# Optimization experiments

Measured on AMD Instinct MI355X. Metric: run time of the kernel, lower is better.

The kernel has to match this reference:

```python
import jax, jax.numpy as jnp
import numpy as np

# ---- fixed architecture hyperparameters (match init_kwargs) ----
B, S = 4, 1024
L, H, DM, DF = 4, 8, 512, 2048
DH = DM // H          # 64 head dim (= 2*R after gated SPE filter)
NS = 5                # num_sines
R = 32                # num_realizations
M = 2 * DH            # favor_feature_dims = 128 (split as +/- of 64 projections)
LN_EPS = 1e-5
ATT_EPS = 1e-6


def layernorm(x, g, b):
    mu = x.mean(-1, keepdims=True)
    var = ((x - mu) ** 2).mean(-1, keepdims=True)
    return (x - mu) * jax.lax.rsqrt(var + LN_EPS) * g + b


def sine_spe(freqs, offsets, gains, noise, seq_len):
    """SineSPE positional code. freqs/offsets/gains: (H,DH,NS); noise: (H,DH,2NS,R).
    Returns qbar, kbar of shape (S,H,DH,R)."""
    pos = jnp.arange(seq_len, dtype=freqs.dtype)
    f = jax.nn.sigmoid(freqs)[:, :, None, :] / 2.0                       # (H,DH,1,NS)
    ph_q = 2.0 * jnp.pi * f * pos[None, None, :, None] + offsets[:, :, None, :]
    ph_k = 2.0 * jnp.pi * f * pos[None, None, :, None]
    om_q = jnp.stack([jnp.cos(ph_q), jnp.sin(ph_q)], -1).reshape(H, DH, seq_len, 2 * NS)
    om_k = jnp.stack([jnp.cos(ph_k), jnp.sin(ph_k)], -1).reshape(H, DH, seq_len, 2 * NS)
    g = jax.nn.softplus(gains)
    g = jnp.stack([g, g], -1).reshape(H, DH, 2 * NS)                      # upsample gains
    z = noise * g[..., None] / jnp.sqrt(jnp.asarray(2.0 * NS, freqs.dtype))
    qbar = jnp.einsum('hdsk,hdkr->shdr', om_q, z)
    kbar = jnp.einsum('hdsk,hdkr->shdr', om_k, z)
    scale = (R * DH) ** 0.25
    return qbar / scale, kbar / scale


def spe_filter(q, k, qbar, kbar, gate, gnoise):
    """Gated SPE filter. q,k: (B,S,H,DH); qbar/kbar: (S,H,DH,R); gate: (H,DH); gnoise: (H,DH,R).
    Returns qhat, khat of shape (B,S,H,2R)."""
    g = jax.nn.sigmoid(gate)[..., None]                                   # (H,DH,1)
    gn = gnoise / (DH * R) ** 0.25
    seq_len = qbar.shape[0]
    bias = jnp.broadcast_to(jnp.sqrt(g) * gn, (seq_len, H, DH, R))
    qb = jnp.concatenate([jnp.sqrt(1.0 - g) * qbar, bias], -1)            # (S,H,DH,2R)
    kb = jnp.concatenate([jnp.sqrt(1.0 - g) * kbar, bias], -1)
    qhat = jnp.einsum('bshd,shdr->bshr', q, qb)
    khat = jnp.einsum('bshd,shdr->bshr', k, kb)
    return qhat, khat


def favor(x, omega):
    """FAVOR+ softmax feature map. x: (B,S,H,DH); omega: (DH, M//2) -> (B,S,H,M)."""
    x = x * (DH ** -0.25)                                                 # sqrt(softmax_temp), temp=1/sqrt(DH)
    half_norm = 0.5 * jnp.sum(x * x, -1, keepdims=True)
    u = jnp.einsum('bshe,em->bshm', x, omega)
    phi = jnp.concatenate([jnp.exp(u - half_norm), jnp.exp(-u - half_norm)], -1)
    return phi / jnp.sqrt(jnp.asarray(M, x.dtype))


def causal_linear_attention(Q, K, V):
    """Causal linear (kernelized) attention via lax.scan. Q,K: (B,S,H,M); V: (B,S,H,DH)."""
    Bv = Q.shape[0]

    def step(carry, qkv):
        Skv, sk = carry
        q, k, v = qkv                                                     # (B,H,M),(B,H,M),(B,H,DH)
        Skv = Skv + jnp.einsum('bhm,bhd->bhmd', k, v)
        sk = sk + k
        num = jnp.einsum('bhm,bhmd->bhd', q, Skv)
        den = jnp.einsum('bhm,bhm->bh', q, sk) + ATT_EPS
        return (Skv, sk), num / den[..., None]

    init = (jnp.zeros((Bv, H, M, DH), Q.dtype), jnp.zeros((Bv, H, M), Q.dtype))
    xs = tuple(jnp.moveaxis(t, 1, 0) for t in (Q, K, V))
    _, out = jax.lax.scan(step, init, xs)
    return jnp.moveaxis(out, 0, 1)                                        # (B,S,H,DH)


def setup_inputs() -> dict:
    key = jax.random.key(0)
    ks = jax.random.split(key, 14)

    def rn(k, shape, scale=1.0):
        return jax.random.normal(k, shape, dtype=jnp.float32) * scale

    return {
        'x': rn(ks[0], (B, S, DM)),
        'Wq': rn(ks[1], (L, DM, DM), 0.02), 'bq': jnp.zeros((L, DM), jnp.float32),
        'Wk': rn(ks[2], (L, DM, DM), 0.02), 'bk': jnp.zeros((L, DM), jnp.float32),
        'Wv': rn(ks[3], (L, DM, DM), 0.02), 'bv': jnp.zeros((L, DM), jnp.float32),
        'Wo': rn(ks[4], (L, DM, DM), 0.02), 'bo': jnp.zeros((L, DM), jnp.float32),
        'W1': rn(ks[5], (L, DM, DF), 0.02), 'b1': jnp.zeros((L, DF), jnp.float32),
        'W2': rn(ks[6], (L, DF, DM), 0.02), 'b2': jnp.zeros((L, DM), jnp.float32),
        'ln1_g': jnp.ones((L, DM), jnp.float32), 'ln1_b': jnp.zeros((L, DM), jnp.float32),
        'ln2_g': jnp.ones((L, DM), jnp.float32), 'ln2_b': jnp.zeros((L, DM), jnp.float32),
        'spe_freqs': rn(ks[7], (L, H, DH, NS)),
        'spe_offsets': rn(ks[8], (L, H, DH, NS)),
        'spe_gains': rn(ks[9], (L, H, DH, NS)),
        'spe_noise': rn(ks[10], (L, H, DH, 2 * NS, R)),
        'gate': rn(ks[11], (L, H, DH)),
        'gate_noise': rn(ks[12], (L, H, DH, R)),
        'favor_omega': rn(ks[13], (L, DH, M // 2)),
    }


def reference(x, Wq, bq, Wk, bk, Wv, bv, Wo, bo, W1, b1, W2, b2,
              ln1_g, ln1_b, ln2_g, ln2_b,
              spe_freqs, spe_offsets, spe_gains, spe_noise, gate, gate_noise, favor_omega):
    Bv, Sv, _ = x.shape
    out = x
    for l in range(L):
        qbar, kbar = sine_spe(spe_freqs[l], spe_offsets[l], spe_gains[l], spe_noise[l], Sv)
        q = (out @ Wq[l] + bq[l]).reshape(Bv, Sv, H, DH)
        k = (out @ Wk[l] + bk[l]).reshape(Bv, Sv, H, DH)
        v = (out @ Wv[l] + bv[l]).reshape(Bv, Sv, H, DH)
        qh, kh = spe_filter(q, k, qbar, kbar, gate[l], gate_noise[l])
        Qf = favor(qh, favor_omega[l])
        Kf = favor(kh, favor_omega[l])
        att = causal_linear_attention(Qf, Kf, v).reshape(Bv, Sv, DM)
        att = att @ Wo[l] + bo[l]
        h = layernorm(out + att, ln1_g[l], ln1_b[l])
        y = jax.nn.relu(h @ W1[l] + b1[l]) @ W2[l] + b2[l]
        out = layernorm(h + y, ln2_g[l], ln2_b[l])
    return out
```

## Files before the change

### kernel.cpp

```cpp
#include <hip/hip_runtime.h>
#include <math.h>

#define BB 4
#define SS 1024
#define LL 4
#define HH 8
#define DM 512
#define DF 2048
#define DH 64
#define NS 5
#define RR 32
#define MM 128
#define NC 16
#define CHK 64
#define QKV_N 1536

#define INV_SQRT10   0.316227766016838f
#define INV_SCALE    0.148650889375340f
#define TEMP_SCALE   0.353553390593274f
#define INV_SQRT_M   0.088388347648318f
#define TWO_PI       6.283185307179586f

typedef __attribute__((ext_vector_type(8))) short bf16x8;
typedef __attribute__((ext_vector_type(4))) float f32x4;

__device__ __forceinline__ unsigned short f2bf(float f) {
  union { float f; unsigned int u; } v; v.f = f;
  unsigned int r = v.u + 0x7FFFu + ((v.u >> 16) & 1u);
  return (unsigned short)(r >> 16);
}

__device__ __forceinline__ float bf2f(unsigned short u) {
  union { unsigned int u; float f; } v; v.u = (unsigned int)u << 16;
  return v.f;
}

__device__ __forceinline__ void gld_lds16(const unsigned short* g, unsigned short* l) {
  __builtin_amdgcn_global_load_lds((const __attribute__((address_space(1))) void*)g,
                                   (__attribute__((address_space(3))) void*)l,
                                   16, 0, 0);
}

template<int RELU, int OUT_BF>
__global__ __launch_bounds__(256)
void gemm_mfma(const unsigned short* __restrict__ A, const unsigned short* __restrict__ Bt,
               const float* __restrict__ bias, float* __restrict__ Cf,
               unsigned short* __restrict__ Cbf, int M, int N, int K)
{
  __shared__ unsigned short As[128 * 32];
  __shared__ unsigned short Bs[128 * 32];
  const int tid  = threadIdx.x;
  const int w    = tid >> 6;
  const int lane = tid & 63;
  const int row0 = blockIdx.y * 128;
  const int col0 = blockIdx.x * 128;
  const int wr = (w >> 1) * 64;
  const int wc = (w & 1) * 64;
  const int c0 = w * 2, c1 = w * 2 + 1;
  const int m0 = c0 * 16 + (lane >> 2);
  const int m1 = c1 * 16 + (lane >> 2);
  const int kA = (lane & 3) * 8;

  f32x4 acc[4][4] = {};

  for (int k0 = 0; k0 < K; k0 += 32) {
    gld_lds16(&A [(size_t)(row0 + m0) * K + k0 + kA], &As[c0 * 512]);
    gld_lds16(&A [(size_t)(row0 + m1) * K + k0 + kA], &As[c1 * 512]);
    gld_lds16(&Bt[(size_t)(col0 + m0) * K + k0 + kA], &Bs[c0 * 512]);
    gld_lds16(&Bt[(size_t)(col0 + m1) * K + k0 + kA], &Bs[c1 * 512]);
    __syncthreads();
    const int rA = wr + (lane & 15);
    const int rB = wc + (lane & 15);
    const int kk = (lane >> 4) * 8;
    bf16x8 af[4], bfr[4];
#pragma unroll
    for (int i = 0; i < 4; ++i) {
      af[i]  = *reinterpret_cast<const bf16x8*>(&As[(rA + i * 16) * 32 + kk]);
      bfr[i] = *reinterpret_cast<const bf16x8*>(&Bs[(rB + i * 16) * 32 + kk]);
    }
#pragma unroll
    for (int mi = 0; mi < 4; ++mi)
#pragma unroll
      for (int ni = 0; ni < 4; ++ni)
        acc[mi][ni] = __builtin_amdgcn_mfma_f32_16x16x32_bf16(af[mi], bfr[ni], acc[mi][ni], 0, 0, 0);
    __syncthreads();
  }
  const int cr = (lane >> 4) * 4;
  const int cc = lane & 15;
#pragma unroll
  for (int mi = 0; mi < 4; ++mi) {
#pragma unroll
    for (int ni = 0; ni < 4; ++ni) {
      const int col = col0 + wc + ni * 16 + cc;
      const float bv = bias[col];
#pragma unroll
      for (int r = 0; r < 4; ++r) {
        const int row = row0 + wr + mi * 16 + cr + r;
        float v = acc[mi][ni][r] + bv;
        if (RELU) v = fmaxf(v, 0.f);
        if (OUT_BF) Cbf[(size_t)row * N + col] = f2bf(v);
        else        Cf [(size_t)row * N + col] = v;
      }
    }
  }
}

template<int RELU, int OUT_BF>
__global__ __launch_bounds__(256)
void gemm_mfma_n64(const unsigned short* __restrict__ A, const unsigned short* __restrict__ Bt,
                   const float* __restrict__ bias, float* __restrict__ Cf,
                   unsigned short* __restrict__ Cbf, int M, int N, int K)
{
  __shared__ unsigned short As[128 * 32];
  __shared__ unsigned short Bs[64 * 32];
  const int tid  = threadIdx.x;
  const int w    = tid >> 6;
  const int lane = tid & 63;
  const int row0 = blockIdx.y * 128;
  const int col0 = blockIdx.x * 64;
  const int wr = (w >> 1) * 64;
  const int wc = (w & 1) * 32;
  const int c0 = w * 2, c1 = w * 2 + 1;
  const int m0 = c0 * 16 + (lane >> 2);
  const int m1 = c1 * 16 + (lane >> 2);
  const int mb = w * 16 + (lane >> 2);
  const int kA = (lane & 3) * 8;

  f32x4 acc[4][2] = {};

  for (int k0 = 0; k0 < K; k0 += 32) {
    gld_lds16(&A [(size_t)(row0 + m0) * K + k0 + kA], &As[c0 * 512]);
    gld_lds16(&A [(size_t)(row0 + m1) * K + k0 + kA], &As[c1 * 512]);
    gld_lds16(&Bt[(size_t)(col0 + mb) * K + k0 + kA], &Bs[w * 512]);
    __syncthreads();
    const int rA = wr + (lane & 15);
    const int rB = wc + (lane & 15);
    const int kk = (lane >> 4) * 8;
    bf16x8 af[4], bfr[2];
#pragma unroll
    for (int i = 0; i < 4; ++i)
      af[i]  = *reinterpret_cast<const bf16x8*>(&As[(rA + i * 16) * 32 + kk]);
#pragma unroll
    for (int i = 0; i < 2; ++i)
      bfr[i] = *reinterpret_cast<const bf16x8*>(&Bs[(rB + i * 16) * 32 + kk]);
#pragma unroll
    for (int mi = 0; mi < 4; ++mi)
#pragma unroll
      for (int ni = 0; ni < 2; ++ni)
        acc[mi][ni] = __builtin_amdgcn_mfma_f32_16x16x32_bf16(af[mi], bfr[ni], acc[mi][ni], 0, 0, 0);
    __syncthreads();
  }
  const int cr = (lane >> 4) * 4;
  const int cc = lane & 15;
#pragma unroll
  for (int mi = 0; mi < 4; ++mi) {
#pragma unroll
    for (int ni = 0; ni < 2; ++ni) {
      const int col = col0 + wc + ni * 16 + cc;
      const float bv = bias[col];
#pragma unroll
      for (int r = 0; r < 4; ++r) {
        const int row = row0 + wr + mi * 16 + cr + r;
        float v = acc[mi][ni][r] + bv;
        if (RELU) v = fmaxf(v, 0.f);
        if (OUT_BF) Cbf[(size_t)row * N + col] = f2bf(v);
        else        Cf [(size_t)row * N + col] = v;
      }
    }
  }
}

__global__ __launch_bounds__(256)
void transpose_bf(const float* __restrict__ W, unsigned short* __restrict__ Wt, int K, int N,
                  size_t inStride, size_t outStride)
{
  const float* Wl = W + blockIdx.z * inStride;
  unsigned short* Wtl = Wt + blockIdx.z * outStride;
  __shared__ float tile[32][33];
  const int k0 = blockIdx.y * 32, n0 = blockIdx.x * 32;
  const int tx = threadIdx.x & 31, ty = threadIdx.x >> 5;
#pragma unroll
  for (int j = 0; j < 4; ++j)
    tile[ty + 8 * j][tx] = Wl[(size_t)(k0 + ty + 8 * j) * N + n0 + tx];
  __syncthreads();
#pragma unroll
  for (int j = 0; j < 4; ++j)
    Wtl[(size_t)(n0 + ty + 8 * j) * K + k0 + tx] = f2bf(tile[tx][ty + 8 * j]);
}

__global__ __launch_bounds__(256)
void pack_bias(const float* __restrict__ bq, const float* __restrict__ bk,
               const float* __restrict__ bv, float* __restrict__ out)
{
  const int l = blockIdx.y;
  const int i = blockIdx.x * 256 + threadIdx.x;
  if (i < QKV_N)
    out[l * QKV_N + i] = (i < 512) ? bq[l * DM + i] : (i < 1024) ? bk[l * DM + i - 512]
                                                                 : bv[l * DM + i - 1024];
}

__global__ __launch_bounds__(256)
void cvt_bf16(const float* __restrict__ in, unsigned short* __restrict__ out, int n4)
{
  const int i = blockIdx.x * 256 + threadIdx.x;
  if (i < n4) {
    const float4 v = reinterpret_cast<const float4*>(in)[i];
    ushort4 o;
    o.x = f2bf(v.x); o.y = f2bf(v.y); o.z = f2bf(v.z); o.w = f2bf(v.w);
    reinterpret_cast<ushort4*>(out)[i] = o;
  }
}

__global__ __launch_bounds__(256)
void spe_prep_all(const float* __restrict__ gains, const float* __restrict__ noise,
                  const float* __restrict__ gate, const float* __restrict__ gnoise,
                  const float* __restrict__ offsets,
                  unsigned short* __restrict__ zpb, unsigned short* __restrict__ wbb,
                  float2* __restrict__ offcs)
{
  const int i = blockIdx.x * 256 + threadIdx.x;
  const int NZ = LL * HH * RR * 10 * DH;
  const int NW = LL * HH * RR * DH;
  const int NO = LL * HH * DH * NS;
  if (i < NZ) {
    const int d = i & 63;
    int j = i >> 6;
    const int k = j % 10; j /= 10;
    const int r = j & 31; j >>= 5;
    const int h = j & 7;  const int l = j >> 3;
    const int lhd = (l * HH + h) * DH + d;
    const float ga = gains[lhd * NS + (k >> 1)];
    const float sp = (ga > 20.f) ? ga : log1pf(__expf(ga));
    const float gg = 1.f / (1.f + __expf(-gate[lhd]));
    const float c1 = sqrtf(fmaxf(1.f - gg, 0.f));
    const float nz = noise[((size_t)lhd * 10 + k) * 32 + r];
    zpb[i] = f2bf(nz * sp * c1 * (INV_SQRT10 * INV_SCALE));
  } else if (i < NZ + NW) {
    int j = i - NZ;
    const int d = j & 63; j >>= 6;
    const int r = j & 31; j >>= 5;
    const int h = j & 7;  const int l = j >> 3;
    const int lhd = (l * HH + h) * DH + d;
    const float gg = 1.f / (1.f + __expf(-gate[lhd]));
    wbb[i - NZ] = f2bf(sqrtf(gg) * gnoise[(size_t)lhd * 32 + r] * INV_SCALE);
  } else if (i < NZ + NW + NO) {
    const int j = i - NZ - NW;
    float sn, cn;
    __sincosf(offsets[j], &sn, &cn);
    offcs[j] = make_float2(cn, sn);
  }
}

__global__ __launch_bounds__(256)
void spe_xhat(const float* __restrict__ freqs, const float2* __restrict__ offcs,
              const unsigned short* __restrict__ zpb, const unsigned short* __restrict__ wbb,
              const float* __restrict__ qkv,
              unsigned short* __restrict__ xhat, float* __restrict__ hn)
{
  const int s = blockIdx.x;
  const int h = blockIdx.y;
  const int t = threadIdx.x;
  const int w = t >> 6;
  const int lane = t & 63;
  __shared__ float omqT[10][64];
  __shared__ float omkT[10][64];
  __shared__ unsigned short qbT[64 * 64];
  __shared__ unsigned short kbT[64 * 64];
  __shared__ unsigned short rQ[16 * 64];
  __shared__ unsigned short rK[16 * 64];
  __shared__ float hqp[4][8];

  for (int e = t; e < DH * NS; e += 256) {
    const int d = e / NS, ns = e - d * NS;
    const float fr = 0.5f / (1.f + __expf(-freqs[(h * DH + d) * NS + ns]));
    float sn, cn;
    __sincosf(TWO_PI * fr * (float)s, &sn, &cn);
    const float2 oc = offcs[(h * DH + d) * NS + ns];
    omkT[2 * ns][d]     = cn;
    omkT[2 * ns + 1][d] = sn;
    omqT[2 * ns][d]     = cn * oc.x - sn * oc.y;
    omqT[2 * ns + 1][d] = sn * oc.x + cn * oc.y;
  }
  {
    const int b = t >> 6, d = t & 63;
    const size_t idx = ((size_t)b * SS + s) * QKV_N + h * DH + d;
    const int sd = d ^ ((b & 7) << 3);
    rQ[b * 64 + sd] = f2bf(qkv[idx] * TEMP_SCALE);
    rK[b * 64 + sd] = f2bf(qkv[idx + 512] * TEMP_SCALE);
  }
  for (int i = t; i < 768; i += 256) {
    rQ[256 + i] = 0;
    rK[256 + i] = 0;
  }
  __syncthreads();
  {
    const int r = t >> 3, dg = t & 7, d0 = dg * 8;
    float accq[8] = {}, acck[8] = {};
    const unsigned short* zr = zpb + (size_t)(h * RR + r) * 10 * 64 + d0;
#pragma unroll
    for (int k = 0; k < 10; ++k) {
      const bf16x8 zv = *reinterpret_cast<const bf16x8*>(zr + (size_t)k * 64);
      const float4 oq0 = *reinterpret_cast<const float4*>(&omqT[k][d0]);
      const float4 oq1 = *reinterpret_cast<const float4*>(&omqT[k][d0 + 4]);
      const float4 ok0 = *reinterpret_cast<const float4*>(&omkT[k][d0]);
      const float4 ok1 = *reinterpret_cast<const float4*>(&omkT[k][d0 + 4]);
      float zf[8];
#pragma unroll
      for (int j = 0; j < 8; ++j) zf[j] = bf2f((unsigned short)zv[j]);
      accq[0] += zf[0] * oq0.x; accq[1] += zf[1] * oq0.y;
      accq[2] += zf[2] * oq0.z; accq[3] += zf[3] * oq0.w;
      accq[4] += zf[4] * oq1.x; accq[5] += zf[5] * oq1.y;
      accq[6] += zf[6] * oq1.z; accq[7] += zf[7] * oq1.w;
      acck[0] += zf[0] * ok0.x; acck[1] += zf[1] * ok0.y;
      acck[2] += zf[2] * ok0.z; acck[3] += zf[3] * ok0.w;
      acck[4] += zf[4] * ok1.x; acck[5] += zf[5] * ok1.y;
      acck[6] += zf[6] * ok1.z; acck[7] += zf[7] * ok1.w;
    }
    bf16x8 qv, kv;
#pragma unroll
    for (int j = 0; j < 8; ++j) {
      qv[j] = (short)f2bf(accq[j]);
      kv[j] = (short)f2bf(acck[j]);
    }
    const int sd0 = d0 ^ ((r & 7) << 3);
    *reinterpret_cast<bf16x8*>(&qbT[r * 64 + sd0]) = qv;
    *reinterpret_cast<bf16x8*>(&kbT[r * 64 + sd0]) = kv;
    const bf16x8 wv = *reinterpret_cast<const bf16x8*>(&wbb[(size_t)(h * RR + r) * 64 + d0]);
    *reinterpret_cast<bf16x8*>(&qbT[(32 + r) * 64 + sd0]) = wv;
    *reinterpret_cast<bf16x8*>(&kbT[(32 + r) * 64 + sd0]) = wv;
  }
  __syncthreads();
  f32x4 aq = {0.f, 0.f, 0.f, 0.f}, ak = {0.f, 0.f, 0.f, 0.f};
  const int arow = lane & 15;
  const int colr = w * 16 + (lane & 15);
#pragma unroll
  for (int kt = 0; kt < 2; ++kt) {
    const int g = kt * 4 + (lane >> 4);
    const bf16x8 fAq = *reinterpret_cast<const bf16x8*>(&rQ[arow * 64 + ((g ^ (arow & 7)) << 3)]);
    const bf16x8 fAk = *reinterpret_cast<const bf16x8*>(&rK[arow * 64 + ((g ^ (arow & 7)) << 3)]);
    const bf16x8 fBq = *reinterpret_cast<const bf16x8*>(&qbT[colr * 64 + ((g ^ (colr & 7)) << 3)]);
    const bf16x8 fBk = *reinterpret_cast<const bf16x8*>(&kbT[colr * 64 + ((g ^ (colr & 7)) << 3)]);
    aq = __builtin_amdgcn_mfma_f32_16x16x32_bf16(fAq, fBq, aq, 0, 0, 0);
    ak = __builtin_amdgcn_mfma_f32_16x16x32_bf16(fAk, fBk, ak, 0, 0, 0);
  }
  float rq[4], rk2[4];
#pragma unroll
  for (int r = 0; r < 4; ++r) { rq[r] = aq[r] * aq[r]; rk2[r] = ak[r] * ak[r]; }
#pragma unroll
  for (int off = 1; off < 16; off <<= 1) {
#pragma unroll
    for (int r = 0; r < 4; ++r) {
      rq[r]  += __shfl_xor(rq[r],  off, 64);
      rk2[r] += __shfl_xor(rk2[r], off, 64);
    }
  }
  if (lane == 0) {
#pragma unroll
    for (int r = 0; r < 4; ++r) { hqp[w][r] = rq[r]; hqp[w][4 + r] = rk2[r]; }
  }
  if (lane < 16) {
#pragma unroll
    for (int r = 0; r < 4; ++r) {
      const size_t rowq = ((size_t)r * SS + s) * HH + h;
      xhat[rowq * 64 + w * 16 + lane] = f2bf(aq[r]);
      xhat[(rowq + (size_t)BB * SS * HH) * 64 + w * 16 + lane] = f2bf(ak[r]);
    }
  }
  __syncthreads();
  if (t < 8) {
    const int b = t & 3;
    const int ko = (t >> 2) * 4;
    const float v = 0.5f * (hqp[0][ko + b] + hqp[1][ko + b] + hqp[2][ko + b] + hqp[3][ko + b]);
    const size_t row = ((size_t)b * SS + s) * HH + h + (size_t)(t >> 2) * BB * SS * HH;
    hn[row] = v;
  }
}

__global__ __launch_bounds__(256)
void favor_gemm(const unsigned short* __restrict__ xhat, const unsigned short* __restrict__ omgT,
                const float* __restrict__ hn, unsigned short* __restrict__ QfKfB)
{
  __shared__ unsigned short As[128 * 32];
  __shared__ unsigned short Bs[64 * 32];
  const int tid  = threadIdx.x;
  const int w    = tid >> 6;
  const int lane = tid & 63;
  const int row0 = blockIdx.x * 128;
  const int c0 = w * 2, c1 = w * 2 + 1;
  const int m0 = c0 * 16 + (lane >> 2);
  const int m1 = c1 * 16 + (lane >> 2);
  const int mb = w * 16 + (lane >> 2);
  const int kA = (lane & 3) * 8;

  f32x4 acc[2][4] = {};

  for (int k0 = 0; k0 < 64; k0 += 32) {
    gld_lds16(&xhat[(size_t)(row0 + m0) * 64 + k0 + kA], &As[c0 * 512]);
    gld_lds16(&xhat[(size_t)(row0 + m1) * 64 + k0 + kA], &As[c1 * 512]);
    gld_lds16(&omgT[(size_t)mb * 64 + k0 + kA], &Bs[w * 512]);
    __syncthreads();
    const int rA = w * 32 + (lane & 15);
    const int kk = (lane >> 4) * 8;
    bf16x8 af[2], bfr[4];
#pragma unroll
    for (int i = 0; i < 2; ++i)
      af[i]  = *reinterpret_cast<const bf16x8*>(&As[(rA + i * 16) * 32 + kk]);
#pragma unroll
    for (int i = 0; i < 4; ++i)
      bfr[i] = *reinterpret_cast<const bf16x8*>(&Bs[(i * 16 + (lane & 15)) * 32 + kk]);
#pragma unroll
    for (int mi = 0; mi < 2; ++mi)
#pragma unroll
      for (int ni = 0; ni < 4; ++ni)
        acc[mi][ni] = __builtin_amdgcn_mfma_f32_16x16x32_bf16(af[mi], bfr[ni], acc[mi][ni], 0, 0, 0);
    __syncthreads();
  }
  const int cr = (lane >> 4) * 4;
  const int cc = lane & 15;
#pragma unroll
  for (int mi = 0; mi < 2; ++mi) {
#pragma unroll
    for (int r = 0; r < 4; ++r) {
      const size_t row = row0 + w * 32 + mi * 16 + cr + r;
      const float hnv = hn[row];
#pragma unroll
      for (int ni = 0; ni < 4; ++ni) {
        const int m = ni * 16 + cc;
        const float u = acc[mi][ni][r];
        QfKfB[row * MM + m]      = f2bf(__expf( u - hnv) * INV_SQRT_M);
        QfKfB[row * MM + m + 64] = f2bf(__expf(-u - hnv) * INV_SQRT_M);
      }
    }
  }
}

__global__ __launch_bounds__(256)
void attn_chunk_sums(const unsigned short* __restrict__ KfB, const float* __restrict__ qkv,
                     float* __restrict__ Sch, float* __restrict__ kch)
{
  const int c = blockIdx.x, h = blockIdx.y, b = blockIdx.z;
  const int tid = threadIdx.x;
  const int w = tid >> 6, lane = tid & 63;
  __shared__ unsigned short KcT[128 * 64];
  __shared__ unsigned short VT[64 * 64];
  const size_t srow0 = (size_t)b * SS + c * CHK;

  for (int i = tid; i < 8192; i += 256) {
    const int m = i & 127, t = i >> 7;
    KcT[m * 64 + (t ^ ((m & 7) << 3))] = KfB[((srow0 + t) * HH + h) * MM + m];
  }
  for (int i = tid; i < 4096; i += 256) {
    const int d = i & 63, tt = i >> 6;
    VT[d * 64 + (tt ^ ((d & 7) << 3))] = f2bf(qkv[(srow0 + tt) * QKV_N + 1024 + h * DH + d]);
  }
  __syncthreads();

  const int kk = (lane >> 4) * 8;
  f32x4 acc[2][4] = {};
#pragma unroll
  for (int kc = 0; kc < 2; ++kc) {
    const int k = kc * 32 + kk;
#pragma unroll
    for (int mi = 0; mi < 2; ++mi) {
      const int mA = w * 32 + mi * 16 + (lane & 15);
      const bf16x8 a = *reinterpret_cast<const bf16x8*>(&KcT[mA * 64 + (k ^ ((mA & 7) << 3))]);
#pragma unroll
      for (int ni = 0; ni < 4; ++ni) {
        const int dB = ni * 16 + (lane & 15);
        const bf16x8 bb = *reinterpret_cast<const bf16x8*>(&VT[dB * 64 + (k ^ ((dB & 7) << 3))]);
        acc[mi][ni] = __builtin_amdgcn_mfma_f32_16x16x32_bf16(a, bb, acc[mi][ni], 0, 0, 0);
      }
    }
  }
  const size_t base = (((size_t)b * HH + h) * NC + c);
  float* So = Sch + base * (MM * DH);
  const int cr = (lane >> 4) * 4, cc = lane & 15;
#pragma unroll
  for (int mi = 0; mi < 2; ++mi)
#pragma unroll
    for (int ni = 0; ni < 4; ++ni)
#pragma unroll
      for (int r = 0; r < 4; ++r)
        So[(size_t)(w * 32 + mi * 16 + cr + r) * DH + ni * 16 + cc] = acc[mi][ni][r];
  {
    const int m = tid >> 1, half = tid & 1;
    float ks = 0.f;
#pragma unroll
    for (int j = 0; j < 32; ++j) {
      const int t2 = half * 32 + j;
      ks += bf2f(KcT[m * 64 + (t2 ^ ((m & 7) << 3))]);
    }
    ks += __shfl_xor(ks, 1, 64);
    if (half == 0) kch[base * MM + m] = ks;
  }
}

__global__ __launch_bounds__(256)
void attn_scan(float* __restrict__ Sch, float* __restrict__ kch)
{
  const int bh = blockIdx.x, part = blockIdx.y;
  const int t = threadIdx.x;
  float* base = Sch + (size_t)bh * NC * (MM * DH);
  for (int e = part * 1024 + t; e < (part + 1) * 1024; e += 256) {
    float run = 0.f;
#pragma unroll
    for (int c = 0; c < NC; ++c) {
      const float v = base[(size_t)c * (MM * DH) + e];
      base[(size_t)c * (MM * DH) + e] = run;
      run += v;
    }
  }
  if (part == 0 && t < MM) {
    float* kb2 = kch + (size_t)bh * NC * MM;
    float run = 0.f;
#pragma unroll
    for (int c = 0; c < NC; ++c) {
      const float v = kb2[c * MM + t];
      kb2[c * MM + t] = run;
      run += v;
    }
  }
}

__global__ __launch_bounds__(256)
void attn_out(const unsigned short* __restrict__ QfKfB, const float* __restrict__ qkv,
              const float* __restrict__ Sch, const float* __restrict__ kch,
              unsigned short* __restrict__ att)
{
  const int c = blockIdx.x, h = blockIdx.y, b = blockIdx.z;
  const int tid = threadIdx.x;
  const int w = tid >> 6;
  const int lane = tid & 63;
  __shared__ unsigned short Qc[64 * 128];
  __shared__ unsigned short Sb[64 * 64];
  __shared__ unsigned short KVU[12288];
  __shared__ float skp[MM];
  __shared__ float denl[64];

  unsigned short* Kc   = KVU;
  unsigned short* SpxT = KVU;
  unsigned short* VT   = KVU + 8192;

  const size_t srow0 = (size_t)b * SS + c * CHK;
  const unsigned short* Qg = QfKfB + (srow0 * HH + h) * MM;
  const unsigned short* Kg = Qg + (size_t)BB * SS * HH * MM;

  if (tid < MM) skp[tid] = kch[(((size_t)b * HH + h) * NC + c) * MM + tid];

  for (int i = tid; i < 1024; i += 256) {
    const int s2 = i >> 4, m8 = (i & 15) * 8;
    const int sw = m8 ^ ((s2 & 15) << 3);
    *reinterpret_cast<bf16x8*>(&Qc[s2 * 128 + sw]) =
        *reinterpret_cast<const bf16x8*>(&Qg[(size_t)s2 * (HH * MM) + m8]);
    *reinterpret_cast<bf16x8*>(&Kc[s2 * 128 + sw]) =
        *reinterpret_cast<const bf16x8*>(&Kg[(size_t)s2 * (HH * MM) + m8]);
  }
  for (int i = tid; i < 4096; i += 256) {
    const int d = i & 63, tt = i >> 6;
    const float v = qkv[(srow0 + tt) * QKV_N + 1024 + h * DH + d];
    VT[d * 64 + (tt ^ ((d & 7) << 3))] = f2bf(v);
  }
  __syncthreads();

  const int sA = w * 16 + (lane & 15);
  const int kk = (lane >> 4) * 8;
  f32x4 acc_s[4] = {};
#pragma unroll
  for (int kc = 0; kc < 4; ++kc) {
    const int k = kc * 32 + kk;
    const bf16x8 aq = *reinterpret_cast<const bf16x8*>(&Qc[sA * 128 + (k ^ ((sA & 15) << 3))]);
#pragma unroll
    for (int n = 0; n < 4; ++n) {
      const int tB = n * 16 + (lane & 15);
      const bf16x8 bq = *reinterpret_cast<const bf16x8*>(&Kc[tB * 128 + (k ^ ((tB & 15) << 3))]);
      acc_s[n] = __builtin_amdgcn_mfma_f32_16x16x32_bf16(aq, bq, acc_s[n], 0, 0, 0);
    }
  }
  __syncthreads();

  {
    const int g = lane >> 4;
    const int tcol = lane & 15;
    float dintra[4] = {0.f, 0.f, 0.f, 0.f};
#pragma unroll
    for (int r = 0; r < 4; ++r) {
      const int s = w * 16 + g * 4 + r;
#pragma unroll
      for (int n = 0; n < 4; ++n) {
        const int t2 = n * 16 + tcol;
        const float v = (t2 <= s) ? acc_s[n][r] : 0.f;
        dintra[r] += v;
        Sb[s * 64 + (t2 ^ ((s & 7) << 3))] = f2bf(v);
      }
    }
#pragma unroll
    for (int off = 1; off < 16; off <<= 1)
#pragma unroll
      for (int r = 0; r < 4; ++r) dintra[r] += __shfl_xor(dintra[r], off, 64);
    if (tcol == 0) {
#pragma unroll
      for (int r = 0; r < 4; ++r) denl[w * 16 + g * 4 + r] = dintra[r];
    }
  }
  {
    const float* Sp = Sch + (((size_t)b * HH + h) * NC + c) * (MM * DH);
    for (int i = tid; i < 8192; i += 256) {
      const int d = i & 63, m = i >> 6;
      SpxT[d * 128 + (m ^ ((d & 15) << 3))] = f2bf(Sp[(size_t)m * DH + d]);
    }
  }
  __syncthreads();

  f32x4 acc_o[4] = {};
#pragma unroll
  for (int kc = 0; kc < 2; ++kc) {
    const int k = kc * 32 + kk;
    const bf16x8 as = *reinterpret_cast<const bf16x8*>(&Sb[sA * 64 + (k ^ ((sA & 7) << 3))]);
#pragma unroll
    for (int n = 0; n < 4; ++n) {
      const int dB = n * 16 + (lane & 15);
      const bf16x8 bv = *reinterpret_cast<const bf16x8*>(&VT[dB * 64 + (k ^ ((dB & 7) << 3))]);
      acc_o[n] = __builtin_amdgcn_mfma_f32_16x16x32_bf16(as, bv, acc_o[n], 0, 0, 0);
    }
  }
#pragma unroll
  for (int kc = 0; kc < 4; ++kc) {
    const int k = kc * 32 + kk;
    const bf16x8 aq = *reinterpret_cast<const bf16x8*>(&Qc[sA * 128 + (k ^ ((sA & 15) << 3))]);
#pragma unroll
    for (int n = 0; n < 4; ++n) {
      const int dB = n * 16 + (lane & 15);
      const bf16x8 bs = *reinterpret_cast<const bf16x8*>(&SpxT[dB * 128 + (k ^ ((dB & 15) << 3))]);
      acc_o[n] = __builtin_amdgcn_mfma_f32_16x16x32_bf16(aq, bs, acc_o[n], 0, 0, 0);
    }
  }
  {
    const int s2 = tid >> 2, part = tid & 3;
    float p = 0.f;
#pragma unroll
    for (int j = 0; j < 32; ++j) {
      const int m = part * 32 + j;
      p += bf2f(Qc[s2 * 128 + (m ^ ((s2 & 15) << 3))]) * skp[m];
    }
    p += __shfl_xor(p, 1, 64);
    p += __shfl_xor(p, 2, 64);
    if (part == 0) denl[s2] += p + 1e-6f;
  }
  __syncthreads();

  {
    const int g = lane >> 4;
    const int dcol = lane & 15;
#pragma unroll
    for (int r = 0; r < 4; ++r) {
      const int s = w * 16 + g * 4 + r;
      const float dinv = 1.f / denl[s];
#pragma unroll
      for (int n = 0; n < 4; ++n)
        att[(srow0 + s) * DM + h * DH + n * 16 + dcol] = f2bf(acc_o[n][r] * dinv);
    }
  }
}

template<int WBF>
__global__ __launch_bounds__(256)
void add_ln(const float* __restrict__ a, const float* __restrict__ bres,
            const float* __restrict__ g, const float* __restrict__ be,
            float* __restrict__ out, unsigned short* __restrict__ outbf)
{
  const int row = blockIdx.x;
  const int t = threadIdx.x;
  const size_t base = (size_t)row * DM;
  const float x0 = a[base + t] + bres[base + t];
  const float x1 = a[base + t + 256] + bres[base + t + 256];
  __shared__ float red[8];
  float ssum = x0 + x1;
#pragma unroll
  for (int off = 32; off > 0; off >>= 1) ssum += __shfl_xor(ssum, off, 64);
  const int wid = t >> 6, lid = t & 63;
  if (lid == 0) red[wid] = ssum;
  __syncthreads();
  const float mu = (red[0] + red[1] + red[2] + red[3]) * (1.f / DM);
  const float d0 = x0 - mu, d1 = x1 - mu;
  float sv = d0 * d0 + d1 * d1;
#pragma unroll
  for (int off = 32; off > 0; off >>= 1) sv += __shfl_xor(sv, off, 64);
  if (lid == 0) red[4 + wid] = sv;
  __syncthreads();
  const float var = (red[4] + red[5] + red[6] + red[7]) * (1.f / DM);
  const float rs = rsqrtf(var + 1e-5f);
  const float o0 = d0 * rs * g[t]       + be[t];
  const float o1 = d1 * rs * g[t + 256] + be[t + 256];
  out[base + t]       = o0;
  out[base + t + 256] = o1;
  if (WBF) {
    outbf[base + t]       = f2bf(o0);
    outbf[base + t + 256] = f2bf(o1);
  }
}

extern "C" void kernel_launch(void* const* d_in, const int* in_sizes, int n_in,
                              void* d_out, int out_size, void* d_ws, size_t ws_size,
                              hipStream_t stream)
{
  const float* x      = (const float*)d_in[0];
  const float* Wq     = (const float*)d_in[1];
  const float* bq     = (const float*)d_in[2];
  const float* Wk     = (const float*)d_in[3];
  const float* bk     = (const float*)d_in[4];
  const float* Wv     = (const float*)d_in[5];
  const float* bv     = (const float*)d_in[6];
  const float* Wo     = (const float*)d_in[7];
  const float* bo     = (const float*)d_in[8];
  const float* W1     = (const float*)d_in[9];
  const float* b1     = (const float*)d_in[10];
  const float* W2     = (const float*)d_in[11];
  const float* b2     = (const float*)d_in[12];
  const float* ln1g   = (const float*)d_in[13];
  const float* ln1b   = (const float*)d_in[14];
  const float* ln2g   = (const float*)d_in[15];
  const float* ln2b   = (const float*)d_in[16];
  const float* freqs  = (const float*)d_in[17];
  const float* offs   = (const float*)d_in[18];
  const float* gains  = (const float*)d_in[19];
  const float* noise  = (const float*)d_in[20];
  const float* gate   = (const float*)d_in[21];
  const float* gnoise = (const float*)d_in[22];
  const float* omega  = (const float*)d_in[23];

  float* ws = (float*)d_ws;
  size_t o = 0;
  float* curf = ws + o; o += (size_t)BB * SS * DM;
  float* qkvf = ws + o; o += (size_t)BB * SS * QKV_N;
  float* Sch  = ws + o; o += (size_t)BB * HH * NC * MM * DH;
  float* kch  = ws + o; o += (size_t)BB * HH * NC * MM;
  float* hn   = ws + o; o += (size_t)2 * BB * SS * HH;
  float* bqkv = ws + o; o += (size_t)LL * QKV_N;
  float2* offcs = (float2*)(ws + o); o += (size_t)LL * HH * DH * NS * 2;
  unsigned short* zpb = (unsigned short*)(ws + o); o += (size_t)LL * HH * RR * 10 * DH / 2;
  unsigned short* QfKfB = (unsigned short*)(ws + o); o += (size_t)2 * BB * SS * HH * MM / 2;
  unsigned short* xhat  = (unsigned short*)(ws + o); o += (size_t)2 * BB * SS * HH * DH / 2;
  unsigned short* attb  = (unsigned short*)(ws + o); o += (size_t)BB * SS * DM / 2;
  unsigned short* h_bf  = (unsigned short*)(ws + o); o += (size_t)BB * SS * DM / 2;
  unsigned short* curbf = (unsigned short*)(ws + o); o += (size_t)BB * SS * DM / 2;
  unsigned short* Wqkvt = (unsigned short*)(ws + o); o += (size_t)LL * QKV_N * DM / 2;
  unsigned short* Wot   = (unsigned short*)(ws + o); o += (size_t)LL * DM * DM / 2;
  unsigned short* W1t   = (unsigned short*)(ws + o); o += (size_t)DF * DM / 2;
  unsigned short* W2t   = (unsigned short*)(ws + o); o += (size_t)DM * DF / 2;
  unsigned short* omgT  = (unsigned short*)(ws + o); o += (size_t)LL * 4096 / 2;
  unsigned short* wbb   = (unsigned short*)(ws + o); o += (size_t)LL * HH * RR * DH / 2;

  float* attp = qkvf;
  float* hbuf = qkvf + (size_t)2 * 1024 * 1024;
  float* ybuf = qkvf + (size_t)4 * 1024 * 1024;
  unsigned short* midbf = QfKfB;
  unsigned short* KfB   = QfKfB + (size_t)BB * SS * HH * MM;

  const int MROWS = BB * SS;

  cvt_bf16<<<(BB * SS * DM / 4 + 255) / 256, 256, 0, stream>>>(x, curbf, BB * SS * DM / 4);
  spe_prep_all<<<2856, 256, 0, stream>>>(gains, noise, gate, gnoise, offs, zpb, wbb, offcs);
  transpose_bf<<<dim3(16, 16, 4), 256, 0, stream>>>(Wq, Wqkvt,                     DM, DM, (size_t)DM * DM, (size_t)QKV_N * DM);
  transpose_bf<<<dim3(16, 16, 4), 256, 0, stream>>>(Wk, Wqkvt + (size_t)512 * DM,  DM, DM, (size_t)DM * DM, (size_t)QKV_N * DM);
  transpose_bf<<<dim3(16, 16, 4), 256, 0, stream>>>(Wv, Wqkvt + (size_t)1024 * DM, DM, DM, (size_t)DM * DM, (size_t)QKV_N * DM);
  transpose_bf<<<dim3(16, 16, 4), 256, 0, stream>>>(Wo, Wot, DM, DM, (size_t)DM * DM, (size_t)DM * DM);
  transpose_bf<<<dim3(2, 2, 4),   256, 0, stream>>>(omega, omgT, DH, MM / 2, (size_t)DH * (MM / 2), 4096);
  pack_bias<<<dim3(6, 4), 256, 0, stream>>>(bq, bk, bv, bqkv);

  for (int l = 0; l < LL; ++l) {
    const float* in = (l == 0) ? x : curf;

    gemm_mfma_n64<0, 0><<<dim3(QKV_N / 64, MROWS / 128), 256, 0, stream>>>(
        curbf, Wqkvt + (size_t)l * QKV_N * DM, bqkv + (size_t)l * QKV_N,
        qkvf, (unsigned short*)nullptr, MROWS, QKV_N, DM);

    spe_xhat<<<dim3(SS, HH), 256, 0, stream>>>(
        freqs + (size_t)l * HH * DH * NS, offcs + (size_t)l * HH * DH * NS,
        zpb + (size_t)l * HH * RR * 10 * DH, wbb + (size_t)l * HH * RR * DH,
        qkvf, xhat, hn);
    favor_gemm<<<dim3(2 * BB * SS * HH / 128), 256, 0, stream>>>(
        xhat, omgT + (size_t)l * 4096, hn, QfKfB);

    attn_chunk_sums<<<dim3(NC, HH, BB), 256, 0, stream>>>(KfB, qkvf, Sch, kch);
    attn_scan<<<dim3(BB * HH, 8), 256, 0, stream>>>(Sch, kch);
    attn_out<<<dim3(NC, HH, BB), 256, 0, stream>>>(QfKfB, qkvf, Sch, kch, attb);

    gemm_mfma_n64<0, 0><<<dim3(DM / 64, MROWS / 128), 256, 0, stream>>>(
        attb, Wot + (size_t)l * DM * DM, bo + (size_t)l * DM,
        attp, (unsigned short*)nullptr, MROWS, DM, DM);

    add_ln<1><<<MROWS, 256, 0, stream>>>(in, attp, ln1g + (size_t)l * DM, ln1b + (size_t)l * DM, hbuf, h_bf);

    transpose_bf<<<dim3(64, 16, 1), 256, 0, stream>>>(W1 + (size_t)l * DM * DF, W1t, DM, DF, 0, 0);
    gemm_mfma<1, 1><<<dim3(DF / 128, MROWS / 128), 256, 0, stream>>>(
        h_bf, W1t, b1 + (size_t)l * DF, (float*)nullptr, midbf, MROWS, DF, DM);
    transpose_bf<<<dim3(16, 64, 1), 256, 0, stream>>>(W2 + (size_t)l * DF * DM, W2t, DF, DM, 0, 0);
    gemm_mfma_n64<0, 0><<<dim3(DM / 64, MROWS / 128), 256, 0, stream>>>(
        midbf, W2t, b2 + (size_t)l * DM, ybuf, (unsigned short*)nullptr, MROWS, DM, DF);

    if (l == LL - 1) {
      add_ln<0><<<MROWS, 256, 0, stream>>>(hbuf, ybuf, ln2g + (size_t)l * DM, ln2b + (size_t)l * DM,
                                           (float*)d_out, (unsigned short*)nullptr);
    } else {
      add_ln<1><<<MROWS, 256, 0, stream>>>(hbuf, ybuf, ln2g + (size_t)l * DM, ln2b + (size_t)l * DM,
                                           curf, curbf);
    }
  }
}
```

Before: 743.0 us.

## Split-K the Wo and W2 GEMMs and hoist FFN weight transposes out of layer loop

The N=512 GEMMs (attention output projection and FFN down projection) now split K in two across blockIdx.z. Each half writes its own fp32 partial slice, and the following add+layernorm kernel sums both slices. The grid doubles from 256 to 512 blocks, which fills the GPU better. The W1/W2 transposes for all layers now run once before the layer loop instead of inside it, at the cost of more workspace. The partial-sum scheme adds extra fp32 write and read traffic, and the y buffer is relocated to the Sch region to hold two slices.

```diff
diff --git a/kernel.cpp b/kernel.cpp
--- a/kernel.cpp
+++ b/kernel.cpp
@@ -105,7 +105,7 @@
   }
 }
 
-template<int RELU, int OUT_BF>
+template<int RELU, int OUT_BF, int SPLITK>
 __global__ __launch_bounds__(256)
 void gemm_mfma_n64(const unsigned short* __restrict__ A, const unsigned short* __restrict__ Bt,
                    const float* __restrict__ bias, float* __restrict__ Cf,
@@ -118,6 +118,9 @@
   const int lane = tid & 63;
   const int row0 = blockIdx.y * 128;
   const int col0 = blockIdx.x * 64;
+  const int kz   = (SPLITK > 1) ? blockIdx.z : 0;
+  const int Ks   = K / SPLITK;
+  const int kbeg = kz * Ks;
   const int wr = (w >> 1) * 64;
   const int wc = (w & 1) * 32;
   const int c0 = w * 2, c1 = w * 2 + 1;
@@ -128,7 +131,7 @@
 
   f32x4 acc[4][2] = {};
 
-  for (int k0 = 0; k0 < K; k0 += 32) {
+  for (int k0 = kbeg; k0 < kbeg + Ks; k0 += 32) {
     gld_lds16(&A [(size_t)(row0 + m0) * K + k0 + kA], &As[c0 * 512]);
     gld_lds16(&A [(size_t)(row0 + m1) * K + k0 + kA], &As[c1 * 512]);
     gld_lds16(&Bt[(size_t)(col0 + mb) * K + k0 + kA], &Bs[w * 512]);
@@ -152,19 +155,20 @@
   }
   const int cr = (lane >> 4) * 4;
   const int cc = lane & 15;
+  float* Cfo = Cf + (size_t)kz * M * N;
 #pragma unroll
   for (int mi = 0; mi < 4; ++mi) {
 #pragma unroll
     for (int ni = 0; ni < 2; ++ni) {
       const int col = col0 + wc + ni * 16 + cc;
-      const float bv = bias[col];
+      const float bv = (kz == 0) ? bias[col] : 0.f;
 #pragma unroll
       for (int r = 0; r < 4; ++r) {
         const int row = row0 + wr + mi * 16 + cr + r;
         float v = acc[mi][ni][r] + bv;
         if (RELU) v = fmaxf(v, 0.f);
         if (OUT_BF) Cbf[(size_t)row * N + col] = f2bf(v);
-        else        Cf [(size_t)row * N + col] = v;
+        else        Cfo[(size_t)row * N + col] = v;
       }
     }
   }
@@ -662,17 +666,21 @@
   }
 }
 
-template<int WBF>
-__global__ __launch_bounds__(256)
-void add_ln(const float* __restrict__ a, const float* __restrict__ bres,
+template<int WBF, int NSUM>
+__global__ __launch_bounds__(256)
+void add_ln(const float* __restrict__ a, const float* __restrict__ bres, size_t sstride,
             const float* __restrict__ g, const float* __restrict__ be,
             float* __restrict__ out, unsigned short* __restrict__ outbf)
 {
   const int row = blockIdx.x;
   const int t = threadIdx.x;
   const size_t base = (size_t)row * DM;
-  const float x0 = a[base + t] + bres[base + t];
-  const float x1 = a[base + t + 256] + bres[base + t + 256];
+  float x0 = a[base + t] + bres[base + t];
+  float x1 = a[base + t + 256] + bres[base + t + 256];
+  if (NSUM == 2) {
+    x0 += bres[sstride + base + t];
+    x1 += bres[sstride + base + t + 256];
+  }
   __shared__ float red[8];
   float ssum = x0 + x1;
 #pragma unroll
@@ -745,14 +753,15 @@
   unsigned short* curbf = (unsigned short*)(ws + o); o += (size_t)BB * SS * DM / 2;
   unsigned short* Wqkvt = (unsigned short*)(ws + o); o += (size_t)LL * QKV_N * DM / 2;
   unsigned short* Wot   = (unsigned short*)(ws + o); o += (size_t)LL * DM * DM / 2;
-  unsigned short* W1t   = (unsigned short*)(ws + o); o += (size_t)DF * DM / 2;
-  unsigned short* W2t   = (unsigned short*)(ws + o); o += (size_t)DM * DF / 2;
+  unsigned short* W1t   = (unsigned short*)(ws + o); o += (size_t)LL * DF * DM / 2;
+  unsigned short* W2t   = (unsigned short*)(ws + o); o += (size_t)LL * DM * DF / 2;
   unsigned short* omgT  = (unsigned short*)(ws + o); o += (size_t)LL * 4096 / 2;
   unsigned short* wbb   = (unsigned short*)(ws + o); o += (size_t)LL * HH * RR * DH / 2;
 
+  const size_t SLICE = (size_t)BB * SS * DM;
   float* attp = qkvf;
-  float* hbuf = qkvf + (size_t)2 * 1024 * 1024;
-  float* ybuf = qkvf + (size_t)4 * 1024 * 1024;
+  float* hbuf = qkvf + 2 * SLICE;
+  float* ybuf = Sch;
   unsigned short* midbf = QfKfB;
   unsigned short* KfB   = QfKfB + (size_t)BB * SS * HH * MM;
 
@@ -764,13 +773,15 @@
   transpose_bf<<<dim3(16, 16, 4), 256, 0, stream>>>(Wk, Wqkvt + (size_t)512 * DM,  DM, DM, (size_t)DM * DM, (size_t)QKV_N * DM);
   transpose_bf<<<dim3(16, 16, 4), 256, 0, stream>>>(Wv, Wqkvt + (size_t)1024 * DM, DM, DM, (size_t)DM * DM, (size_t)QKV_N * DM);
   transpose_bf<<<dim3(16, 16, 4), 256, 0, stream>>>(Wo, Wot, DM, DM, (size_t)DM * DM, (size_t)DM * DM);
+  transpose_bf<<<dim3(64, 16, 4), 256, 0, stream>>>(W1, W1t, DM, DF, (size_t)DM * DF, (size_t)DF * DM);
+  transpose_bf<<<dim3(16, 64, 4), 256, 0, stream>>>(W2, W2t, DF, DM, (size_t)DF * DM, (size_t)DM * DF);
   transpose_bf<<<dim3(2, 2, 4),   256, 0, stream>>>(omega, omgT, DH, MM / 2, (size_t)DH * (MM / 2), 4096);
   pack_bias<<<dim3(6, 4), 256, 0, stream>>>(bq, bk, bv, bqkv);
 
   for (int l = 0; l < LL; ++l) {
     const float* in = (l == 0) ? x : curf;
 
-    gemm_mfma_n64<0, 0><<<dim3(QKV_N / 64, MROWS / 128), 256, 0, stream>>>(
+    gemm_mfma_n64<0, 0, 1><<<dim3(QKV_N / 64, MROWS / 128), 256, 0, stream>>>(
         curbf, Wqkvt + (size_t)l * QKV_N * DM, bqkv + (size_t)l * QKV_N,
         qkvf, (unsigned short*)nullptr, MROWS, QKV_N, DM);
 
@@ -785,25 +796,26 @@
     attn_scan<<<dim3(BB * HH, 8), 256, 0, stream>>>(Sch, kch);
     attn_out<<<dim3(NC, HH, BB), 256, 0, stream>>>(QfKfB, qkvf, Sch, kch, attb);
 
-    gemm_mfma_n64<0, 0><<<dim3(DM / 64, MROWS / 128), 256, 0, stream>>>(
+    gemm_mfma_n64<0, 0, 2><<<dim3(DM / 64, MROWS / 128, 2), 256, 0, stream>>>(
         attb, Wot + (size_t)l * DM * DM, bo + (size_t)l * DM,
         attp, (unsigned short*)nullptr, MROWS, DM, DM);
 
-    add_ln<1><<<MROWS, 256, 0, stream>>>(in, attp, ln1g + (size_t)l * DM, ln1b + (size_t)l * DM, hbuf, h_bf);
-
-    transpose_bf<<<dim3(64, 16, 1), 256, 0, stream>>>(W1 + (size_t)l * DM * DF, W1t, DM, DF, 0, 0);
+    add_ln<1, 2><<<MROWS, 256, 0, stream>>>(in, attp, SLICE,
+        ln1g + (size_t)l * DM, ln1b + (size_t)l * DM, hbuf, h_bf);
+
     gemm_mfma<1, 1><<<dim3(DF / 128, MROWS / 128), 256, 0, stream>>>(
-        h_bf, W1t, b1 + (size_t)l * DF, (float*)nullptr, midbf, MROWS, DF, DM);
-    transpose_bf<<<dim3(16, 64, 1), 256, 0, stream>>>(W2 + (size_t)l * DF * DM, W2t, DF, DM, 0, 0);
-    gemm_mfma_n64<0, 0><<<dim3(DM / 64, MROWS / 128), 256, 0, stream>>>(
-        midbf, W2t, b2 + (size_t)l * DM, ybuf, (unsigned short*)nullptr, MROWS, DM, DF);
+        h_bf, W1t + (size_t)l * DF * DM, b1 + (size_t)l * DF, (float*)nullptr, midbf, MROWS, DF, DM);
+
+    gemm_mfma_n64<0, 0, 2><<<dim3(DM / 64, MROWS / 128, 2), 256, 0, stream>>>(
+        midbf, W2t + (size_t)l * DM * DF, b2 + (size_t)l * DM,
+        ybuf, (unsigned short*)nullptr, MROWS, DM, DF);
 
     if (l == LL - 1) {
-      add_ln<0><<<MROWS, 256, 0, stream>>>(hbuf, ybuf, ln2g + (size_t)l * DM, ln2b + (size_t)l * DM,
-                                           (float*)d_out, (unsigned short*)nullptr);
+      add_ln<0, 2><<<MROWS, 256, 0, stream>>>(hbuf, ybuf, SLICE,
+          ln2g + (size_t)l * DM, ln2b + (size_t)l * DM, (float*)d_out, (unsigned short*)nullptr);
     } else {
-      add_ln<1><<<MROWS, 256, 0, stream>>>(hbuf, ybuf, ln2g + (size_t)l * DM, ln2b + (size_t)l * DM,
-                                           curf, curbf);
-    }
-  }
-}
+      add_ln<1, 2><<<MROWS, 256, 0, stream>>>(hbuf, ybuf, SLICE,
+          ln2g + (size_t)l * DM, ln2b + (size_t)l * DM, curf, curbf);
+    }
+  }
+}
```

After: 708.8 us. 4.6% less time.
